# Kernel optimization log

Measured on AMD Instinct MI355X. Metric: run time of the kernel, lower is better.

## Reference

```python
import jax, jax.numpy as jnp
import numpy as np

VOCAB = 100000
EMB = 128
D = 8
K = 128
SUB = EMB // D  # 16
BN_EPS = 1e-3  # keras BatchNormalization default epsilon


def setup_inputs() -> dict:
    key = jax.random.key(0)
    k1, k2, k3 = jax.random.split(key, 3)
    ids = jax.random.randint(k1, (1024, 128), 0, VOCAB, dtype=jnp.int64)
    query_wemb = jax.random.normal(k2, (VOCAB, EMB), dtype=jnp.float32)
    centroids = jax.random.normal(k3, (D, K, SUB), dtype=jnp.float32)
    return {"ids": ids, "query_wemb": query_wemb, "centroids": centroids}


def reference(ids, query_wemb, centroids):
    d, k, sub = centroids.shape
    emb = d * sub
    flat = ids.reshape(-1)                      # [N]
    x = query_wemb[flat].reshape(-1, d, sub)    # [N, d, sub]

    norm_x = jnp.sum(x * x, axis=-1, keepdims=True)          # [N, d, 1]
    norm_c = jnp.sum(centroids * centroids, axis=-1)[None]   # [1, d, k]
    dot = jnp.einsum('nds,dks->ndk', x, centroids)           # [N, d, k]
    response = -norm_x + 2.0 * dot - norm_c                  # [N, d, k]

    # BatchNorm(scale=False, center=False), training=True: batch stats over
    # axes (0,1), per-k channel (keras default axis=-1)
    mean = jnp.mean(response, axis=(0, 1), keepdims=True)
    var = jnp.var(response, axis=(0, 1), keepdims=True)
    resp_bn = (response - mean) * jax.lax.rsqrt(var + BN_EPS)

    codes = jnp.argmax(resp_bn, axis=-1)                     # [N, d]

    # per-subspace centroid gather (non-shared centroids)
    outputs = centroids[jnp.arange(d)[None, :], codes]       # [N, d, sub]

    # straight-through estimator
    out_st = x + jax.lax.stop_gradient(outputs - x)          # [N, d, sub]
    return out_st.reshape(ids.shape + (emb,))
```

## Files before the change

kernel.cpp:

```cpp
#include <hip/hip_runtime.h>


constexpr int NTOK = 131072;
constexpr int ST   = 2320;
constexpr float EPS = 0.001f;

typedef float v2f __attribute__((ext_vector_type(2)));


__global__ __launch_bounds__(256) void k1_stats(const int* __restrict__ ids,
                                                const float* __restrict__ wemb,
                                                float* __restrict__ partials,
                                                int tpb)
{
    __shared__ float xs[32][132];
    __shared__ float nrm[32][8];
    const int t = threadIdx.x;
    const int b = blockIdx.x;

    float g[4][4];
#pragma unroll
    for (int i = 0; i < 4; ++i)
#pragma unroll
        for (int j = 0; j < 4; ++j) g[i][j] = 0.f;
    float sx = 0.f, hh = 0.f, s2 = 0.f;

    const int d_g = t >> 4;
    const int r0  = ((t >> 2) & 3) << 2;
    const int c0  = (t & 3) << 2;
    const int u   = t & 127;
    const int d_s = u >> 4;
    const int s_s = u & 15;

    const int nchunks = tpb >> 5;
    for (int ch = 0; ch < nchunks; ++ch) {
        const int n0 = b * tpb + ch * 32;
#pragma unroll
        for (int rep = 0; rep < 4; ++rep) {
            int i = t + rep * 256;
            int n = i >> 5, f = i & 31;
            int id = ids[n0 + n];
            float4 v = *(const float4*)(wemb + (size_t)id * 128 + f * 4);
            *(float4*)(&xs[n][f * 4]) = v;
        }
        __syncthreads();
        {
            int n = t >> 3, dd = t & 7;
            const float* xp = &xs[n][dd * 16];
            float4 a = *(const float4*)(xp);
            float4 bq = *(const float4*)(xp + 4);
            float4 c = *(const float4*)(xp + 8);
            float4 dq = *(const float4*)(xp + 12);
            float acc = a.x*a.x + a.y*a.y + a.z*a.z + a.w*a.w;
            acc += bq.x*bq.x + bq.y*bq.y + bq.z*bq.z + bq.w*bq.w;
            acc += c.x*c.x + c.y*c.y + c.z*c.z + c.w*c.w;
            acc += dq.x*dq.x + dq.y*dq.y + dq.z*dq.z + dq.w*dq.w;
            nrm[n][dd] = acc;
        }
        __syncthreads();
        if (t < 128) {
            for (int n = 0; n < 32; ++n) {
                const float* xp = &xs[n][d_g * 16];
                float4 av = *(const float4*)(xp + r0);
                float4 bv = *(const float4*)(xp + c0);
                float aa[4] = {av.x, av.y, av.z, av.w};
                float bb[4] = {bv.x, bv.y, bv.z, bv.w};
#pragma unroll
                for (int i = 0; i < 4; ++i)
#pragma unroll
                    for (int j = 0; j < 4; ++j)
                        g[i][j] = fmaf(aa[i], bb[j], g[i][j]);
            }
        } else {
            for (int n = 0; n < 32; ++n) {
                float xv = xs[n][d_s * 16 + s_s];
                float nv = nrm[n][d_s];
                sx += xv;
                hh = fmaf(nv, xv, hh);
                if (s_s == 0) s2 = fmaf(nv, nv, s2);
            }
        }
        __syncthreads();
    }
    float* pb = partials + (size_t)b * ST;
    if (t < 128) {
        const int base = d_g * 256;
#pragma unroll
        for (int i = 0; i < 4; ++i)
#pragma unroll
            for (int j = 0; j < 4; ++j)
                pb[base + (r0 + i) * 16 + (c0 + j)] = g[i][j];
    } else {
        pb[2048 + d_s * 16 + s_s] = sx;
        pb[2176 + d_s * 16 + s_s] = hh;
        if (s_s == 0) pb[2304 + d_s] = s2;
    }
}

__global__ __launch_bounds__(256) void k2a_reduce(float* __restrict__ partials, int nb)
{
    const int idx = blockIdx.x * 256 + threadIdx.x;
    if (idx >= 2312) return;
    const int y = blockIdx.y;
    float acc[8] = {0.f, 0.f, 0.f, 0.f, 0.f, 0.f, 0.f, 0.f};
    int b = y;
    while (b + 7 * 32 < nb) {
#pragma unroll
        for (int u = 0; u < 8; ++u)
            acc[u] += partials[(size_t)(b + u * 32) * ST + idx];
        b += 8 * 32;
    }
    while (b < nb) { acc[0] += partials[(size_t)b * ST + idx]; b += 32; }
    float s = ((acc[0] + acc[1]) + (acc[2] + acc[3]))
            + ((acc[4] + acc[5]) + (acc[6] + acc[7]));
    partials[(size_t)y * ST + idx] = s;
}

__global__ __launch_bounds__(256) void k2b_reduce(const float* __restrict__ partials,
                                                  float* __restrict__ stats)
{
    const int idx = blockIdx.x * 256 + threadIdx.x;
    if (idx >= 2312) return;
    float acc[8] = {0.f, 0.f, 0.f, 0.f, 0.f, 0.f, 0.f, 0.f};
#pragma unroll
    for (int j = 0; j < 4; ++j)
#pragma unroll
        for (int u = 0; u < 8; ++u)
            acc[u] += partials[(size_t)(j * 8 + u) * ST + idx];
    stats[idx] = ((acc[0] + acc[1]) + (acc[2] + acc[3]))
               + ((acc[4] + acc[5]) + (acc[6] + acc[7]));
}

__global__ __launch_bounds__(128) void k3_final(const float* __restrict__ stats,
                                                const float* __restrict__ centroids,
                                                float2* __restrict__ ab)
{
    __shared__ float st[2312];
    const int t = threadIdx.x;
    for (int i = t; i < 2312; i += 128) st[i] = stats[i];
    __syncthreads();
    const int k = t;

    double Sn[8], Sn_tot = 0.0, S2_tot = 0.0;
#pragma unroll
    for (int d = 0; d < 8; ++d) {
        double s = 0.0;
        for (int ss = 0; ss < 16; ++ss) s += (double)st[d * 256 + ss * 17];
        Sn[d] = s; Sn_tot += s;
        S2_tot += (double)st[2304 + d];
    }
    double sr = -Sn_tot, sr2 = S2_tot;
    double ncd[8];
    for (int d = 0; d < 8; ++d) {
        const float* cp = centroids + d * 2048 + k * 16;
        float cv[16];
#pragma unroll
        for (int s = 0; s < 16; ++s) cv[s] = cp[s];
        double nc = 0, cdSx = 0, ch = 0, cGc = 0;
        for (int s = 0; s < 16; ++s) {
            nc   += (double)cv[s] * cv[s];
            cdSx += (double)cv[s] * st[2048 + d * 16 + s];
            ch   += (double)cv[s] * st[2176 + d * 16 + s];
            double rd = 0;
            for (int s2i = 0; s2i < 16; ++s2i)
                rd += (double)st[d * 256 + s * 16 + s2i] * cv[s2i];
            cGc += (double)cv[s] * rd;
        }
        ncd[d] = nc;
        sr  += 2.0 * cdSx - (double)NTOK * nc;
        sr2 += 4.0 * cGc + (double)NTOK * nc * nc + 2.0 * nc * Sn[d]
               - 4.0 * ch - 4.0 * nc * cdSx;
    }
    const double M = (double)NTOK * 8.0;
    double mean = sr / M;
    double var  = sr2 / M - mean * mean;
    float alpha = (float)(1.0 / sqrt(var + (double)EPS));
#pragma unroll
    for (int d = 0; d < 8; ++d) {
        float beta = (float)((double)alpha * (-ncd[d] - mean));
        ab[d * 128 + k] = make_float2(2.f * alpha, beta);
    }
}

__global__ __launch_bounds__(256, 4) void k4_main(const int* __restrict__ ids,
                                                  const float* __restrict__ wemb,
                                                  const float* __restrict__ centroids,
                                                  const float2* __restrict__ ab,
                                                  float* __restrict__ out)
{
    __shared__ float  cs[128 * 16];
    __shared__ float2 gbs[128];

    const int t = threadIdx.x;
    const int d = blockIdx.y;
    const float* cd = centroids + (size_t)d * 2048;

#pragma unroll
    for (int i = 0; i < 2; ++i)
        ((float4*)cs)[t + i * 256] = ((const float4*)cd)[t + i * 256];
    if (t < 128) gbs[t] = ab[(size_t)d * 128 + t];

    const int nbase = blockIdx.x * 1024 + t;
    v2f x[4][8];
    v2f nxv[4];
    float best[4];
    int   code[4];
#pragma unroll
    for (int j = 0; j < 4; ++j) {
        const int n = nbase + j * 256;
        const float* xp = wemb + (size_t)ids[n] * 128 + d * 16;
#pragma unroll
        for (int q = 0; q < 4; ++q) {
            float4 v = *(const float4*)(xp + q * 4);
            x[j][q * 2]     = (v2f){v.x, v.y};
            x[j][q * 2 + 1] = (v2f){v.z, v.w};
        }
        float s = 0.f;
#pragma unroll
        for (int q = 0; q < 8; ++q)
            s += x[j][q][0] * x[j][q][0] + x[j][q][1] * x[j][q][1];
        nxv[j] = (v2f){-0.5f * s, 0.f};
        best[j] = -3.4e38f;
        code[j] = 0;
    }

    __syncthreads();

#pragma unroll 2
    for (int k = 0; k < 128; ++k) {
        const float4 c0 = *(const float4*)(&cs[k * 16 + 0]);
        const float4 c1 = *(const float4*)(&cs[k * 16 + 4]);
        const float4 c2 = *(const float4*)(&cs[k * 16 + 8]);
        const float4 c3 = *(const float4*)(&cs[k * 16 + 12]);
        const float2 g  = gbs[k];
        const v2f cc0 = (v2f){c0.x, c0.y}, cc1 = (v2f){c0.z, c0.w};
        const v2f cc2 = (v2f){c1.x, c1.y}, cc3 = (v2f){c1.z, c1.w};
        const v2f cc4 = (v2f){c2.x, c2.y}, cc5 = (v2f){c2.z, c2.w};
        const v2f cc6 = (v2f){c3.x, c3.y}, cc7 = (v2f){c3.z, c3.w};
#pragma unroll
        for (int j = 0; j < 4; ++j) {
            v2f a = __builtin_elementwise_fma(cc0, x[j][0], nxv[j]);
            a = __builtin_elementwise_fma(cc1, x[j][1], a);
            a = __builtin_elementwise_fma(cc2, x[j][2], a);
            a = __builtin_elementwise_fma(cc3, x[j][3], a);
            a = __builtin_elementwise_fma(cc4, x[j][4], a);
            a = __builtin_elementwise_fma(cc5, x[j][5], a);
            a = __builtin_elementwise_fma(cc6, x[j][6], a);
            a = __builtin_elementwise_fma(cc7, x[j][7], a);
            float acc = a[0] + a[1];
            float sc = fmaf(g.x, acc, g.y);
            bool p = sc > best[j];
            best[j] = p ? sc : best[j];
            code[j] = p ? k : code[j];
        }
    }

#pragma unroll
    for (int j = 0; j < 4; ++j) {
        const int n = nbase + j * 256;
        const float* cw = &cs[code[j] * 16];
        float* op = out + (size_t)n * 128 + d * 16;
#pragma unroll
        for (int q = 0; q < 4; ++q) {
            float4 cv = *(const float4*)(cw + q * 4);
            float x0 = x[j][q * 2][0],     x1 = x[j][q * 2][1];
            float x2 = x[j][q * 2 + 1][0], x3 = x[j][q * 2 + 1][1];
            float4 o;
            o.x = x0 + (cv.x - x0);
            o.y = x1 + (cv.y - x1);
            o.z = x2 + (cv.z - x2);
            o.w = x3 + (cv.w - x3);
            *(float4*)(op + q * 4) = o;
        }
    }
}

extern "C" void kernel_launch(void* const* d_in, const int* in_sizes, int n_in,
                              void* d_out, int out_size, void* d_ws, size_t ws_size,
                              hipStream_t stream)
{
    const int* ids    = (const int*)d_in[0];
    const float* wemb = (const float*)d_in[1];
    const float* cent = (const float*)d_in[2];
    float* out = (float*)d_out;
    float* ws  = (float*)d_ws;

    int p1b = 1024;
    if (ws_size < ((size_t)1024 * ST + 2320 + 2048) * 4) p1b = 512;
    if (ws_size < ((size_t)512  * ST + 2320 + 2048) * 4) p1b = 256;
    if (ws_size < ((size_t)256  * ST + 2320 + 2048) * 4) p1b = 128;
    const int tpb = NTOK / p1b;

    float* partials = ws;
    float* stats    = ws + (size_t)p1b * ST;
    float2* ab      = (float2*)(stats + 2320);

    hipLaunchKernelGGL(k1_stats,   dim3(p1b),     dim3(256), 0, stream, ids, wemb, partials, tpb);
    hipLaunchKernelGGL(k2a_reduce, dim3(10, 32),  dim3(256), 0, stream, partials, p1b);
    hipLaunchKernelGGL(k2b_reduce, dim3(10),      dim3(256), 0, stream, partials, stats);
    hipLaunchKernelGGL(k3_final,   dim3(1),       dim3(128), 0, stream, stats, cent, ab);
    hipLaunchKernelGGL(k4_main,    dim3(128, 8),  dim3(256), 0, stream, ids, wemb, cent, ab, out);
}
```

Baseline: 121.6 us.

## Process 8 tokens per thread and software-pipeline centroid LDS reads in main kernel

The main argmax kernel now gives each thread 8 tokens instead of 4 and halves the grid, so each centroid row read from LDS is reused across twice as many dot products. Centroid and scale/bias reads for the next k are issued through inline ds_read asm one iteration ahead, with an explicit wait and scheduling barrier, so LDS latency overlaps with the FMAs. The -0.5||x||^2 term moves out of the packed accumulator into a scalar add, and the final output gather reads centroids from global memory rather than LDS. Register use roughly doubles and the launch-bounds occupancy hint is dropped, which may lower occupancy and hurt hiding of the initial gather latency.

```diff
diff --git a/kernel.cpp b/kernel.cpp
--- a/kernel.cpp
+++ b/kernel.cpp
@@ -182,11 +182,11 @@
     }
 }
 
-__global__ __launch_bounds__(256, 4) void k4_main(const int* __restrict__ ids,
-                                                  const float* __restrict__ wemb,
-                                                  const float* __restrict__ centroids,
-                                                  const float2* __restrict__ ab,
-                                                  float* __restrict__ out)
+__global__ __launch_bounds__(256) void k4_main(const int* __restrict__ ids,
+                                               const float* __restrict__ wemb,
+                                               const float* __restrict__ centroids,
+                                               const float2* __restrict__ ab,
+                                               float* __restrict__ out)
 {
     __shared__ float  cs[128 * 16];
     __shared__ float2 gbs[128];
@@ -200,46 +200,57 @@
         ((float4*)cs)[t + i * 256] = ((const float4*)cd)[t + i * 256];
     if (t < 128) gbs[t] = ab[(size_t)d * 128 + t];
 
-    const int nbase = blockIdx.x * 1024 + t;
-    v2f x[4][8];
-    v2f nxv[4];
-    float best[4];
-    int   code[4];
-#pragma unroll
-    for (int j = 0; j < 4; ++j) {
+    const int nbase = blockIdx.x * 2048 + t;
+    v2f x[8][8];
+    float nx[8], best[8];
+    int   code[8];
+#pragma unroll
+    for (int j = 0; j < 8; ++j) {
         const int n = nbase + j * 256;
         const float* xp = wemb + (size_t)ids[n] * 128 + d * 16;
+        float s = 0.f;
 #pragma unroll
         for (int q = 0; q < 4; ++q) {
             float4 v = *(const float4*)(xp + q * 4);
             x[j][q * 2]     = (v2f){v.x, v.y};
             x[j][q * 2 + 1] = (v2f){v.z, v.w};
-        }
-        float s = 0.f;
-#pragma unroll
-        for (int q = 0; q < 8; ++q)
-            s += x[j][q][0] * x[j][q][0] + x[j][q][1] * x[j][q][1];
-        nxv[j] = (v2f){-0.5f * s, 0.f};
+            s += v.x * v.x + v.y * v.y + v.z * v.z + v.w * v.w;
+        }
+        nx[j] = -0.5f * s;
         best[j] = -3.4e38f;
         code[j] = 0;
     }
 
     __syncthreads();
 
+    const unsigned cs_base = (unsigned)(unsigned long long)(const void*)&cs[0];
+    const unsigned gb_base = (unsigned)(unsigned long long)(const void*)&gbs[0];
+
+    float4 c0 = *(const float4*)(&cs[0]);
+    float4 c1 = *(const float4*)(&cs[4]);
+    float4 c2 = *(const float4*)(&cs[8]);
+    float4 c3 = *(const float4*)(&cs[12]);
+    float2 g  = gbs[0];
+
 #pragma unroll 2
     for (int k = 0; k < 128; ++k) {
-        const float4 c0 = *(const float4*)(&cs[k * 16 + 0]);
-        const float4 c1 = *(const float4*)(&cs[k * 16 + 4]);
-        const float4 c2 = *(const float4*)(&cs[k * 16 + 8]);
-        const float4 c3 = *(const float4*)(&cs[k * 16 + 12]);
-        const float2 g  = gbs[k];
+        const unsigned kn = (unsigned)((k + 1) & 127);
+        const unsigned ra = cs_base + kn * 64;
+        const unsigned rg = gb_base + kn * 8;
+        float4 m0, m1, m2, m3;
+        float2 mg;
+        asm volatile("ds_read_b128 %0, %1"           : "=v"(m0) : "v"(ra));
+        asm volatile("ds_read_b128 %0, %1 offset:16" : "=v"(m1) : "v"(ra));
+        asm volatile("ds_read_b128 %0, %1 offset:32" : "=v"(m2) : "v"(ra));
+        asm volatile("ds_read_b128 %0, %1 offset:48" : "=v"(m3) : "v"(ra));
+        asm volatile("ds_read_b64  %0, %1"           : "=v"(mg) : "v"(rg));
         const v2f cc0 = (v2f){c0.x, c0.y}, cc1 = (v2f){c0.z, c0.w};
         const v2f cc2 = (v2f){c1.x, c1.y}, cc3 = (v2f){c1.z, c1.w};
         const v2f cc4 = (v2f){c2.x, c2.y}, cc5 = (v2f){c2.z, c2.w};
         const v2f cc6 = (v2f){c3.x, c3.y}, cc7 = (v2f){c3.z, c3.w};
 #pragma unroll
-        for (int j = 0; j < 4; ++j) {
-            v2f a = __builtin_elementwise_fma(cc0, x[j][0], nxv[j]);
+        for (int j = 0; j < 8; ++j) {
+            v2f a = __builtin_elementwise_fma(cc0, x[j][0], (v2f){0.f, 0.f});
             a = __builtin_elementwise_fma(cc1, x[j][1], a);
             a = __builtin_elementwise_fma(cc2, x[j][2], a);
             a = __builtin_elementwise_fma(cc3, x[j][3], a);
@@ -247,18 +258,21 @@
             a = __builtin_elementwise_fma(cc5, x[j][5], a);
             a = __builtin_elementwise_fma(cc6, x[j][6], a);
             a = __builtin_elementwise_fma(cc7, x[j][7], a);
-            float acc = a[0] + a[1];
+            float acc = (a[0] + a[1]) + nx[j];
             float sc = fmaf(g.x, acc, g.y);
             bool p = sc > best[j];
             best[j] = p ? sc : best[j];
             code[j] = p ? k : code[j];
         }
-    }
-
-#pragma unroll
-    for (int j = 0; j < 4; ++j) {
+        asm volatile("s_waitcnt lgkmcnt(0)");
+        __builtin_amdgcn_sched_barrier(0);
+        c0 = m0; c1 = m1; c2 = m2; c3 = m3; g = mg;
+    }
+
+#pragma unroll
+    for (int j = 0; j < 8; ++j) {
         const int n = nbase + j * 256;
-        const float* cw = &cs[code[j] * 16];
+        const float* cw = cd + code[j] * 16;
         float* op = out + (size_t)n * 128 + d * 16;
 #pragma unroll
         for (int q = 0; q < 4; ++q) {
@@ -299,5 +313,5 @@
     hipLaunchKernelGGL(k2a_reduce, dim3(10, 32),  dim3(256), 0, stream, partials, p1b);
     hipLaunchKernelGGL(k2b_reduce, dim3(10),      dim3(256), 0, stream, partials, stats);
     hipLaunchKernelGGL(k3_final,   dim3(1),       dim3(128), 0, stream, stats, cent, ab);
-    hipLaunchKernelGGL(k4_main,    dim3(128, 8),  dim3(256), 0, stream, ids, wemb, cent, ab, out);
-}
+    hipLaunchKernelGGL(k4_main,    dim3(64, 8),   dim3(256), 0, stream, ids, wemb, cent, ab, out);
+}
```

Measured after the change: 133.7 us. 9.9% more time.

## Software-pipeline centroid LDS reads with inline asm and readlane BN coefficients

Applied to the files above, without the earlier changes.

The k4 inner loop is rewritten as a manually double-buffered pipeline. Inline-asm ds_read_b128 loads for the next centroid are issued before the current centroid's FMAs, with an explicit lgkmcnt wait. The per-k BN scale and bias now sit in registers and are broadcast with readlane instead of being read from shared memory. The final centroid gather reads from global memory rather than LDS. The aim is to hide LDS latency and cut LDS traffic, at the cost of fragile asm, sched barriers that limit compiler scheduling, and a full lgkmcnt(0) drain every step.

```diff
diff --git a/kernel.cpp b/kernel.cpp
--- a/kernel.cpp
+++ b/kernel.cpp
@@ -6,6 +6,10 @@
 constexpr float EPS = 0.001f;
 
 typedef float v2f __attribute__((ext_vector_type(2)));
+
+__device__ inline float rlane(float v, int lane) {
+    return __int_as_float(__builtin_amdgcn_readlane(__float_as_int(v), lane));
+}
 
 
 __global__ __launch_bounds__(256) void k1_stats(const int* __restrict__ ids,
@@ -188,8 +192,7 @@
                                                   const float2* __restrict__ ab,
                                                   float* __restrict__ out)
 {
-    __shared__ float  cs[128 * 16];
-    __shared__ float2 gbs[128];
+    __shared__ __align__(16) float cs[128 * 16];
 
     const int t = threadIdx.x;
     const int d = blockIdx.y;
@@ -198,67 +201,101 @@
 #pragma unroll
     for (int i = 0; i < 2; ++i)
         ((float4*)cs)[t + i * 256] = ((const float4*)cd)[t + i * 256];
-    if (t < 128) gbs[t] = ab[(size_t)d * 128 + t];
+
+    const int lane = t & 63;
+    const float2 g_lo = ab[(size_t)d * 128 + lane];
+    const float2 g_hi = ab[(size_t)d * 128 + 64 + lane];
 
     const int nbase = blockIdx.x * 1024 + t;
     v2f x[4][8];
-    v2f nxv[4];
-    float best[4];
+    float nx[4], best[4];
     int   code[4];
 #pragma unroll
     for (int j = 0; j < 4; ++j) {
         const int n = nbase + j * 256;
         const float* xp = wemb + (size_t)ids[n] * 128 + d * 16;
+        float s = 0.f;
 #pragma unroll
         for (int q = 0; q < 4; ++q) {
             float4 v = *(const float4*)(xp + q * 4);
             x[j][q * 2]     = (v2f){v.x, v.y};
             x[j][q * 2 + 1] = (v2f){v.z, v.w};
-        }
-        float s = 0.f;
-#pragma unroll
-        for (int q = 0; q < 8; ++q)
-            s += x[j][q][0] * x[j][q][0] + x[j][q][1] * x[j][q][1];
-        nxv[j] = (v2f){-0.5f * s, 0.f};
+            s += v.x * v.x + v.y * v.y + v.z * v.z + v.w * v.w;
+        }
+        nx[j] = -0.5f * s;
         best[j] = -3.4e38f;
         code[j] = 0;
     }
 
     __syncthreads();
 
-#pragma unroll 2
-    for (int k = 0; k < 128; ++k) {
-        const float4 c0 = *(const float4*)(&cs[k * 16 + 0]);
-        const float4 c1 = *(const float4*)(&cs[k * 16 + 4]);
-        const float4 c2 = *(const float4*)(&cs[k * 16 + 8]);
-        const float4 c3 = *(const float4*)(&cs[k * 16 + 12]);
-        const float2 g  = gbs[k];
-        const v2f cc0 = (v2f){c0.x, c0.y}, cc1 = (v2f){c0.z, c0.w};
-        const v2f cc2 = (v2f){c1.x, c1.y}, cc3 = (v2f){c1.z, c1.w};
-        const v2f cc4 = (v2f){c2.x, c2.y}, cc5 = (v2f){c2.z, c2.w};
-        const v2f cc6 = (v2f){c3.x, c3.y}, cc7 = (v2f){c3.z, c3.w};
-#pragma unroll
-        for (int j = 0; j < 4; ++j) {
-            v2f a = __builtin_elementwise_fma(cc0, x[j][0], nxv[j]);
-            a = __builtin_elementwise_fma(cc1, x[j][1], a);
-            a = __builtin_elementwise_fma(cc2, x[j][2], a);
-            a = __builtin_elementwise_fma(cc3, x[j][3], a);
-            a = __builtin_elementwise_fma(cc4, x[j][4], a);
-            a = __builtin_elementwise_fma(cc5, x[j][5], a);
-            a = __builtin_elementwise_fma(cc6, x[j][6], a);
-            a = __builtin_elementwise_fma(cc7, x[j][7], a);
-            float acc = a[0] + a[1];
-            float sc = fmaf(g.x, acc, g.y);
-            bool p = sc > best[j];
-            best[j] = p ? sc : best[j];
-            code[j] = p ? k : code[j];
-        }
-    }
+    const unsigned cs_base = (unsigned)(unsigned long long)(const void*)&cs[0];
+
+    float4 A0 = *(const float4*)(&cs[0]);
+    float4 A1 = *(const float4*)(&cs[4]);
+    float4 A2 = *(const float4*)(&cs[8]);
+    float4 A3 = *(const float4*)(&cs[12]);
+    float4 B0, B1, B2, B3;
+
+#define COMPUTE(R0, R1, R2, R3, KK)                                          \
+    {                                                                        \
+        const int kk_ = (KK);                                                \
+        const int kl_ = kk_ & 63;                                            \
+        const float ga_ = rlane(kk_ < 64 ? g_lo.x : g_hi.x, kl_);            \
+        const float gb_ = rlane(kk_ < 64 ? g_lo.y : g_hi.y, kl_);            \
+        const v2f cc0 = (v2f){R0.x, R0.y}, cc1 = (v2f){R0.z, R0.w};          \
+        const v2f cc2 = (v2f){R1.x, R1.y}, cc3 = (v2f){R1.z, R1.w};          \
+        const v2f cc4 = (v2f){R2.x, R2.y}, cc5 = (v2f){R2.z, R2.w};          \
+        const v2f cc6 = (v2f){R3.x, R3.y}, cc7 = (v2f){R3.z, R3.w};          \
+        _Pragma("unroll")                                                    \
+        for (int j = 0; j < 4; ++j) {                                        \
+            v2f a = __builtin_elementwise_fma(cc0, x[j][0], (v2f){0.f,0.f}); \
+            a = __builtin_elementwise_fma(cc1, x[j][1], a);                  \
+            a = __builtin_elementwise_fma(cc2, x[j][2], a);                  \
+            a = __builtin_elementwise_fma(cc3, x[j][3], a);                  \
+            a = __builtin_elementwise_fma(cc4, x[j][4], a);                  \
+            a = __builtin_elementwise_fma(cc5, x[j][5], a);                  \
+            a = __builtin_elementwise_fma(cc6, x[j][6], a);                  \
+            a = __builtin_elementwise_fma(cc7, x[j][7], a);                  \
+            float acc = (a[0] + a[1]) + nx[j];                               \
+            float sc = fmaf(ga_, acc, gb_);                                  \
+            bool p = sc > best[j];             \
+            best[j] = p ? sc : best[j];                                      \
+            code[j] = p ? kk_ : code[j];                                     \
+        }                                                                    \
+    }
+
+#define ISSUE(R0, R1, R2, R3, KK)                                            \
+    {                                                                        \
+        const unsigned ra_ = cs_base + (unsigned)(((KK) & 127) * 64);        \
+        asm volatile("ds_read_b128 %0, %1"           : "=v"(R0) : "v"(ra_)); \
+        asm volatile("ds_read_b128 %0, %1 offset:16" : "=v"(R1) : "v"(ra_)); \
+        asm volatile("ds_read_b128 %0, %1 offset:32" : "=v"(R2) : "v"(ra_)); \
+        asm volatile("ds_read_b128 %0, %1 offset:48" : "=v"(R3) : "v"(ra_)); \
+    }
+
+#define DRAIN()                                                              \
+    __builtin_amdgcn_sched_barrier(0);                                       \
+    asm volatile("s_waitcnt lgkmcnt(0)");                                    \
+    __builtin_amdgcn_sched_barrier(0);
+
+#pragma unroll 1
+    for (int k = 0; k < 128; k += 2) {
+        ISSUE(B0, B1, B2, B3, k + 1)
+        COMPUTE(A0, A1, A2, A3, k)
+        DRAIN()
+        ISSUE(A0, A1, A2, A3, k + 2)
+        COMPUTE(B0, B1, B2, B3, k + 1)
+        DRAIN()
+    }
+#undef COMPUTE
+#undef ISSUE
+#undef DRAIN
 
 #pragma unroll
     for (int j = 0; j < 4; ++j) {
         const int n = nbase + j * 256;
-        const float* cw = &cs[code[j] * 16];
+        const float* cw = cd + code[j] * 16;
         float* op = out + (size_t)n * 128 + d * 16;
 #pragma unroll
         for (int q = 0; q < 4; ++q) {
```

Measured after the change: 129.2 us. 1.06x slower.
